# Kernel tuning notes

Measured on AMD Instinct MI355X. Metric: run time of the kernel, lower is better.

## Reference

```python
import jax, jax.numpy as jnp
import numpy as np

DIM = 384
HEADS = 6
HD = DIM // HEADS
PATCH = 2
FR = 0.5
HEXP = int(HEADS * 4.0)       # attn_proj expanded heads
PR = DIM // 4                  # SQA proj1 out dim
HID = DIM * 4                  # MLP hidden
EPS = 1e-5
SCALE = 1.0 / np.sqrt(HD).astype(np.float32)


def _ln(x, w, b):
    m = jnp.mean(x, axis=-1, keepdims=True)
    v = jnp.var(x, axis=-1, keepdims=True)
    return (x - m) / jnp.sqrt(v + EPS) * w + b


def _lin(x, w, b):
    return x @ w.T + b


def setup_inputs() -> dict:
    key = jax.random.key(0)
    ks = jax.random.split(key, 16)
    def p(i, shape, s=0.02):
        return jax.random.normal(ks[i], shape, jnp.float32) * s
    return {
        "x": jax.random.normal(ks[0], (3136, DIM), jnp.float32),
        "qa": jax.random.normal(ks[1], (1, DIM), jnp.float32),
        "conv_w": p(2, (DIM, 1, 3, 3), 0.1),
        "conv_b": jnp.zeros((DIM,), jnp.float32),
        "norm1_w": jnp.ones((DIM,), jnp.float32),
        "norm1_b": jnp.zeros((DIM,), jnp.float32),
        "norm2_w": jnp.ones((DIM,), jnp.float32),
        "norm2_b": jnp.zeros((DIM,), jnp.float32),
        "qkv_w": p(3, (3 * DIM, DIM)),
        "qkv_b": jnp.zeros((3 * DIM,), jnp.float32),
        "mproj_w": p(4, (DIM, DIM)),
        "mproj_b": jnp.zeros((DIM,), jnp.float32),
        "ap1_w": p(5, (HEXP, HEADS), 0.1),
        "ap1_b": jnp.zeros((HEXP,), jnp.float32),
        "ap2_w": p(6, (HEADS, HEXP), 0.1),
        "ap2_b": jnp.zeros((HEADS,), jnp.float32),
        "kv_w": p(7, (2 * DIM, DIM)),
        "kv_b": jnp.zeros((2 * DIM,), jnp.float32),
        "sp1_w": p(8, (PR, DIM)),
        "sp1_b": jnp.zeros((PR,), jnp.float32),
        "sp2_w": p(9, (DIM, PR)),
        "sp2_b": jnp.zeros((DIM,), jnp.float32),
        "pn_w": jnp.ones((PR,), jnp.float32),
        "pn_b": jnp.zeros((PR,), jnp.float32),
        "fc1_w": p(10, (HID, DIM)),
        "fc1_b": jnp.zeros((HID,), jnp.float32),
        "fc2_w": p(11, (DIM, HID)),
        "fc2_b": jnp.zeros((DIM,), jnp.float32),
    }


def _mmsa(x, qkv_w, qkv_b, mproj_w, mproj_b, ap1_w, ap1_b, ap2_w, ap2_b):
    # x: [S, DIM]
    s = x.shape[0]
    qkv = _lin(x, qkv_w, qkv_b).reshape(s, 3, HEADS, HD).transpose(1, 2, 0, 3)  # [3,h,s,d]
    q, k, v = qkv[0], qkv[1], qkv[2]
    attn = jnp.einsum('hqd,hkd->hqk', q, k) * SCALE           # [h,q,k]
    a = attn.transpose(1, 2, 0)                                # [q,k,h]
    a = a @ ap1_w.T + ap1_b                                    # [q,k,hexp]
    a = jax.nn.softmax(a, axis=1)                              # softmax over k (axis=1)
    a = a @ ap2_w.T + ap2_b                                    # [q,k,h]
    attn = a.transpose(2, 0, 1)                                # [h,q,k]
    out = jnp.einsum('hqk,hkd->hqd', attn, v)
    out = out.transpose(1, 0, 2).reshape(s, DIM)
    return _lin(out, mproj_w, mproj_b)


def _sqa(x, q, kv_w, kv_b, sp1_w, sp1_b, sp2_w, sp2_b, pn_w, pn_b):
    # x: [S, DIM], q: [1, DIM]
    s = x.shape[0]
    qh = q.reshape(1, HEADS, HD).transpose(1, 0, 2)            # [h,1,d]
    kv = _lin(x, kv_w, kv_b).reshape(s, 2, HEADS, HD).transpose(1, 2, 0, 3)
    k, v = kv[0], kv[1]
    attn = jax.nn.softmax(jnp.einsum('hqd,hkd->hqk', qh, k) * SCALE, axis=-1)
    x1 = jnp.einsum('hqk,hkd->hqd', attn, v).transpose(1, 0, 2).reshape(1, DIM)
    x1 = jax.nn.relu(_ln(_lin(x1, sp1_w, sp1_b), pn_w, pn_b))
    x1 = _lin(x1, sp2_w, sp2_b)
    return x + x1                                              # broadcast residual over S


def reference(x, qa, conv_w, conv_b, norm1_w, norm1_b, norm2_w, norm2_b,
              qkv_w, qkv_b, mproj_w, mproj_b, ap1_w, ap1_b, ap2_w, ap2_b,
              kv_w, kv_b, sp1_w, sp1_b, sp2_w, sp2_b, pn_w, pn_b,
              fc1_w, fc1_b, fc2_w, fc2_b):
    L = x.shape[0]
    Hs = int(np.sqrt(L)); Ws = Hs
    # PosCNN2D: depthwise 3x3 conv + residual
    xi = x.T.reshape(1, DIM, Hs, Ws)
    conv = jax.lax.conv_general_dilated(xi, conv_w, (1, 1), 'SAME', feature_group_count=DIM)
    xi = conv + conv_b[None, :, None, None] + xi
    c = xi[0]                                                  # [DIM,Hs,Ws]
    hp, wp = Hs // PATCH, Ws // PATCH
    # 'c (h h1) (w w1) -> (h w) (h1 w1) c'
    x1 = c.reshape(DIM, hp, PATCH, wp, PATCH).transpose(1, 3, 2, 4, 0).reshape(hp * wp, PATCH * PATCH, DIM)
    n = hp * wp
    nf = int(n * FR)
    means = x1.mean(axis=(1, 2))
    idx = jnp.argsort(-means)                                  # descending
    nf_idx, nb_idx = idx[:nf], idx[nf:]
    f = x1[nf_idx].reshape(nf * PATCH * PATCH, DIM)
    b = x1[nb_idx].reshape((n - nf) * PATCH * PATCH, DIM)
    qf = _mmsa(jnp.concatenate([qa, f], axis=0),
               qkv_w, qkv_b, mproj_w, mproj_b, ap1_w, ap1_b, ap2_w, ap2_b)
    qa2, f = qf[:1], qf[1:]
    b = _sqa(b, qa2, kv_w, kv_b, sp1_w, sp1_b, sp2_w, sp2_b, pn_w, pn_b)
    # scatter foreground/background back to patch order
    x1n = jnp.zeros_like(x1)
    x1n = x1n.at[nf_idx].set(f.reshape(nf, PATCH * PATCH, DIM))
    x1n = x1n.at[nb_idx].set(b.reshape(n - nf, PATCH * PATCH, DIM))
    # inverse rearrange '(h w) (h1 w1) c -> ((h h1)(w w1)) c'
    x1f = x1n.reshape(hp, wp, PATCH, PATCH, DIM).transpose(0, 2, 1, 3, 4).reshape(L, DIM)
    x = x + _ln(x1f, norm1_w, norm1_b)
    h = _ln(x, norm2_w, norm2_b)
    h = jax.nn.silu(_lin(h, fc1_w, fc1_b))
    x = x + _lin(h, fc2_w, fc2_b)
    return x, qa2
```

## Files before the change

### kernel.cpp

```cpp
#include <hip/hip_runtime.h>
#include <hip/hip_bf16.h>

#define DIM 384
#define HEADS 6
#define HD 64
#define LPIX 3136
#define HS 56
#define NPATCH 784
#define NF 392
#define SEQ 1569
#define BROWS 1568
#define HEXP 24
#define PR 96
#define HID 1536
#define SCALE 0.125f
#define EPSV 1e-5f
#define KPAD 1576
#define QSTR 9456

typedef short short8v __attribute__((ext_vector_type(8)));
typedef float f32x4 __attribute__((ext_vector_type(4)));
typedef unsigned short ushort;

__device__ __forceinline__ ushort f2b(float f) {
    __hip_bfloat16 h = __float2bfloat16(f);
    return reinterpret_cast<ushort&>(h);
}
__device__ __forceinline__ float b2f(ushort u) {
    unsigned int ui = ((unsigned int)u) << 16;
    return __uint_as_float(ui);
}

struct CvtSeg { const float* s; ushort* d; int n; };
__global__ __launch_bounds__(256) void cvt_kernel(CvtSeg a, CvtSeg b, CvtSeg c, CvtSeg d, CvtSeg e) {
    CvtSeg seg;
    switch (blockIdx.y) { case 0: seg = a; break; case 1: seg = b; break; case 2: seg = c; break;
                          case 3: seg = d; break; default: seg = e; break; }
    int idx = (blockIdx.x * 256 + threadIdx.x) * 8;
    if (idx >= seg.n) return;
    float4 f0 = *reinterpret_cast<const float4*>(seg.s + idx);
    float4 f1 = *reinterpret_cast<const float4*>(seg.s + idx + 4);
    ushort u[8] = { f2b(f0.x), f2b(f0.y), f2b(f0.z), f2b(f0.w),
                    f2b(f1.x), f2b(f1.y), f2b(f1.z), f2b(f1.w) };
    *reinterpret_cast<uint4*>(seg.d + idx) = *reinterpret_cast<uint4*>(u);
}

__global__ __launch_bounds__(384) void conv_kernel(const float* __restrict__ x,
                                                   const float* __restrict__ cw,
                                                   const float* __restrict__ cb,
                                                   float* __restrict__ x1,
                                                   float* __restrict__ means) {
    int l = blockIdx.x, c = threadIdx.x;
    int wid = c >> 6, lane = c & 63;
    int hh = l / HS, ww = l % HS;
    float acc = x[(long)l * DIM + c] + cb[c];
    #pragma unroll
    for (int kh = 0; kh < 3; kh++) {
        int h2 = hh + kh - 1;
        if (h2 < 0 || h2 >= HS) continue;
        #pragma unroll
        for (int kw = 0; kw < 3; kw++) {
            int w2 = ww + kw - 1;
            if (w2 < 0 || w2 >= HS) continue;
            acc += x[((long)h2 * HS + w2) * DIM + c] * cw[c * 9 + kh * 3 + kw];
        }
    }
    int p = (hh >> 1) * 28 + (ww >> 1);
    int t = ((hh & 1) << 1) | (ww & 1);
    x1[(long)(p * 4 + t) * DIM + c] = acc;
    float s = acc;
    #pragma unroll
    for (int off = 32; off >= 1; off >>= 1) s += __shfl_xor(s, off);
    __shared__ float wred[6];
    if (lane == 0) wred[wid] = s;
    __syncthreads();
    if (c == 0) atomicAdd(&means[p], wred[0] + wred[1] + wred[2] + wred[3] + wred[4] + wred[5]);
}

__global__ __launch_bounds__(1024) void partition_kernel(const float* __restrict__ means, int* __restrict__ isfg,
                                                         int* __restrict__ pos, int* __restrict__ fgmap,
                                                         int* __restrict__ bgmap) {
    __shared__ float m_s[NPATCH];
    __shared__ unsigned char flag_s[NPATCH];
    __shared__ int scan_s[256];
    int tid = threadIdx.x;
    if (tid < NPATCH) m_s[tid] = means[tid];
    __syncthreads();
    if (tid < NPATCH) {
        float m = m_s[tid];
        int rank = 0;
        for (int q2 = 0; q2 < NPATCH; q2++) {
            float mq = m_s[q2];
            rank += (mq > m) || (mq == m && q2 < tid);
        }
        flag_s[tid] = (rank < NF) ? 1 : 0;
    }
    __syncthreads();
    if (tid < 256) {
        int base = tid * 4, cnt = 0;
        #pragma unroll
        for (int i = 0; i < 4; i++) { int p = base + i; if (p < NPATCH) cnt += flag_s[p]; }
        scan_s[tid] = cnt;
    }
    __syncthreads();
    for (int off = 1; off < 256; off <<= 1) {
        int add = 0;
        if (tid < 256 && tid >= off) add = scan_s[tid - off];
        __syncthreads();
        if (tid < 256) scan_s[tid] += add;
        __syncthreads();
    }
    if (tid < 256) {
        int base = tid * 4, cnt = 0;
        #pragma unroll
        for (int i = 0; i < 4; i++) { int p = base + i; if (p < NPATCH) cnt += flag_s[p]; }
        int run = scan_s[tid] - cnt;
        for (int i = 0; i < 4; i++) {
            int p = base + i;
            if (p >= NPATCH) break;
            int f = flag_s[p];
            if (f) { isfg[p] = 1; pos[p] = run; fgmap[run] = p; run++; }
            else   { isfg[p] = 0; pos[p] = p - run; bgmap[p - run] = p; }
        }
    }
}

__global__ __launch_bounds__(384) void gather_kernel(const float* __restrict__ x1, const float* __restrict__ qa,
                                                     const int* __restrict__ fgmap, const int* __restrict__ bgmap,
                                                     ushort* __restrict__ Xmsa_bf, float* __restrict__ B,
                                                     ushort* __restrict__ B_bf) {
    int c = threadIdx.x;
    int bid = blockIdx.x;
    if (bid == 0) { Xmsa_bf[c] = f2b(qa[c]); return; }
    if (bid <= BROWS) {
        int r = bid - 1;
        int src = fgmap[r >> 2] * 4 + (r & 3);
        Xmsa_bf[(long)bid * DIM + c] = f2b(x1[(long)src * DIM + c]);
    } else {
        int r = bid - SEQ;
        int src = bgmap[r >> 2] * 4 + (r & 3);
        float v = x1[(long)src * DIM + c];
        B[(long)r * DIM + c] = v;
        B_bf[(long)r * DIM + c] = f2b(v);
    }
}

template<int BM, int BN, int BK, int OPB, int ACT, int OUTBF>
__global__ __launch_bounds__(256) void mgemm(
    const ushort* __restrict__ A, int lda, long long sA,
    const ushort* __restrict__ B, int ldb, long long sB,
    const float* __restrict__ bias, const float* __restrict__ resid, int ldr,
    void* __restrict__ Cv, int ldc, long long sC,
    int M, int N, int K, float alpha) {
    constexpr int LDT = BK + 8;
    constexpr int WR = (BM == 128 && BN == 128) ? 2 : ((BM == 128) ? 4 : 2);
    constexpr int WC = 4 / WR;
    constexpr int MFR = BM / WR / 16;
    constexpr int NFR = BN / WC / 16;
    constexpr int KH = BK / 32;
    __shared__ ushort As[BM * LDT];
    __shared__ ushort Bs[BN * LDT];
    int tid = threadIdx.x;
    int wid = tid >> 6, lane = tid & 63;
    int m0 = blockIdx.y * BM, n0 = blockIdx.x * BN;
    int bz = blockIdx.z;
    A += (long long)bz * sA;
    B += (long long)bz * sB;
    int wm = (wid / WC) * (BM / WR);
    int wn = (wid % WC) * (BN / WC);
    f32x4 acc[MFR][NFR];
    #pragma unroll
    for (int mi = 0; mi < MFR; mi++)
        #pragma unroll
        for (int ni = 0; ni < NFR; ni++) acc[mi][ni] = (f32x4){0.f, 0.f, 0.f, 0.f};

    for (int k0 = 0; k0 < K; k0 += BK) {
        {
            constexpr int CPR = BK / 8;
            constexpr int CHA = BM * CPR / 256;
            #pragma unroll
            for (int t = 0; t < CHA; t++) {
                int chunk = tid + t * 256;
                int row = chunk / CPR, part = chunk % CPR;
                int gm = m0 + row, gk = k0 + part * 8;
                ushort* dst = &As[row * LDT + part * 8];
                if (gm < M && gk + 8 <= K) {
                    *reinterpret_cast<uint4*>(dst) =
                        *reinterpret_cast<const uint4*>(&A[(long long)gm * lda + gk]);
                } else {
                    #pragma unroll
                    for (int i = 0; i < 8; i++) {
                        int k = gk + i;
                        dst[i] = (gm < M && k < K) ? A[(long long)gm * lda + k] : (ushort)0;
                    }
                }
            }
        }
        if (OPB == 1) {
            constexpr int CPR = BK / 8;
            constexpr int CHB = BN * CPR / 256;
            #pragma unroll
            for (int t = 0; t < CHB; t++) {
                int chunk = tid + t * 256;
                int row = chunk / CPR, part = chunk % CPR;
                int gn = n0 + row, gk = k0 + part * 8;
                ushort* dst = &Bs[row * LDT + part * 8];
                if (gn < N && gk + 8 <= K) {
                    *reinterpret_cast<uint4*>(dst) =
                        *reinterpret_cast<const uint4*>(&B[(long long)gn * ldb + gk]);
                } else {
                    #pragma unroll
                    for (int i = 0; i < 8; i++) {
                        int k = gk + i;
                        dst[i] = (gn < N && k < K) ? B[(long long)gn * ldb + k] : (ushort)0;
                    }
                }
            }
        } else {
            int kr = tid >> 2, nn = (tid & 3) * 16;
            int gk = k0 + kr;
            ushort vals[16];
            if (gk < K && n0 + nn + 16 <= N) {
                *reinterpret_cast<uint4*>(vals) =
                    *reinterpret_cast<const uint4*>(&B[(long long)gk * ldb + n0 + nn]);
                *reinterpret_cast<uint4*>(vals + 8) =
                    *reinterpret_cast<const uint4*>(&B[(long long)gk * ldb + n0 + nn + 8]);
            } else {
                #pragma unroll
                for (int i = 0; i < 16; i++) {
                    int gn = n0 + nn + i;
                    vals[i] = (gk < K && gn < N) ? B[(long long)gk * ldb + gn] : (ushort)0;
                }
            }
            #pragma unroll
            for (int i = 0; i < 16; i++) Bs[(nn + i) * LDT + kr] = vals[i];
        }
        __syncthreads();
        #pragma unroll
        for (int kh = 0; kh < KH; kh++) {
            short8v a[MFR], b[NFR];
            int kcol = kh * 32 + (lane >> 4) * 8;
            #pragma unroll
            for (int mi = 0; mi < MFR; mi++)
                a[mi] = *reinterpret_cast<const short8v*>(&As[(wm + mi * 16 + (lane & 15)) * LDT + kcol]);
            #pragma unroll
            for (int ni = 0; ni < NFR; ni++)
                b[ni] = *reinterpret_cast<const short8v*>(&Bs[(wn + ni * 16 + (lane & 15)) * LDT + kcol]);
            #pragma unroll
            for (int mi = 0; mi < MFR; mi++)
                #pragma unroll
                for (int ni = 0; ni < NFR; ni++)
                    acc[mi][ni] = __builtin_amdgcn_mfma_f32_16x16x32_bf16(a[mi], b[ni], acc[mi][ni], 0, 0, 0);
        }
        __syncthreads();
    }
    ushort* C16 = (ushort*)Cv;
    float* C32 = (float*)Cv;
    #pragma unroll
    for (int mi = 0; mi < MFR; mi++) {
        #pragma unroll
        for (int j = 0; j < 4; j++) {
            int gm = m0 + wm + mi * 16 + (lane >> 4) * 4 + j;
            if (gm >= M) continue;
            #pragma unroll
            for (int ni = 0; ni < NFR; ni++) {
                int gn = n0 + wn + ni * 16 + (lane & 15);
                if (gn >= N) continue;
                float v = acc[mi][ni][j] * alpha;
                if (bias) v += bias[gn];
                if (ACT == 1) v = v / (1.f + __expf(-v));
                if (resid) v += resid[(long long)gm * ldr + gn];
                long long ci = bz * sC + (long long)gm * ldc + gn;
                if (OUTBF) C16[ci] = f2b(v); else C32[ci] = v;
            }
        }
    }
}

__global__ __launch_bounds__(512, 2) void modattn_kernel(
    ushort* __restrict__ S,
    const float* __restrict__ ap1_w, const float* __restrict__ ap1_b,
    const float* __restrict__ ap2_w, const float* __restrict__ ap2_b) {
    int q = blockIdx.x, tid = threadIdx.x;
    int wid = tid >> 6, lane = tid & 63;
    __shared__ ushort s_lds[6 * KPAD];
    __shared__ float w1s[144], w2s[144], b1s[24], b2s[6];
    __shared__ float red[8][12];
    __shared__ float fin[12];
    if (tid < 144) { w1s[tid] = ap1_w[tid]; w2s[tid] = ap2_w[tid]; }
    if (tid < 24) b1s[tid] = ap1_b[tid];
    if (tid < 6)  b2s[tid] = ap2_b[tid];
    {
        const uint4* g = reinterpret_cast<const uint4*>(S + (long long)q * QSTR);
        uint4* l = reinterpret_cast<uint4*>(s_lds);
        #pragma unroll
        for (int t = 0; t < 3; t++) {
            int i = tid + t * 512;
            if (i < 1182) l[i] = g[i];
        }
    }
    __syncthreads();
    float a2acc[4][6];
    #pragma unroll
    for (int j = 0; j < 4; j++)
        #pragma unroll
        for (int h = 0; h < 6; h++) a2acc[j][h] = b2s[h];

    #pragma unroll
    for (int c = 0; c < 2; c++) {
        float a1[4][12];
        float r12[12];
        #pragma unroll
        for (int e = 0; e < 12; e++) r12[e] = -3.4e38f;
        #pragma unroll
        for (int j = 0; j < 4; j++) {
            int k = tid + j * 512;
            bool val = k < SEQ;
            int kc = val ? k : 0;
            float sv[6];
            #pragma unroll
            for (int h = 0; h < 6; h++) sv[h] = b2f(s_lds[h * KPAD + kc]);
            #pragma unroll
            for (int e = 0; e < 12; e++) {
                int eg = c * 12 + e;
                float a = b1s[eg];
                #pragma unroll
                for (int h = 0; h < 6; h++) a = fmaf(sv[h], w1s[eg * 6 + h], a);
                a1[j][e] = a;
                if (val) r12[e] = fmaxf(r12[e], a);
            }
        }
        #pragma unroll
        for (int e = 0; e < 12; e++) {
            float v = r12[e];
            #pragma unroll
            for (int off = 32; off >= 1; off >>= 1) v = fmaxf(v, __shfl_xor(v, off));
            r12[e] = v;
        }
        if (lane == 0) {
            #pragma unroll
            for (int e = 0; e < 12; e++) red[wid][e] = r12[e];
        }
        __syncthreads();
        if (tid < 12) {
            float v = red[0][tid];
            #pragma unroll
            for (int w = 1; w < 8; w++) v = fmaxf(v, red[w][tid]);
            fin[tid] = v;
        }
        __syncthreads();
        #pragma unroll
        for (int e = 0; e < 12; e++) r12[e] = 0.f;
        #pragma unroll
        for (int j = 0; j < 4; j++) {
            int k = tid + j * 512;
            bool val = k < SEQ;
            #pragma unroll
            for (int e = 0; e < 12; e++) {
                float p = val ? __expf(a1[j][e] - fin[e]) : 0.f;
                a1[j][e] = p;
                r12[e] += p;
            }
        }
        #pragma unroll
        for (int e = 0; e < 12; e++) {
            float v = r12[e];
            #pragma unroll
            for (int off = 32; off >= 1; off >>= 1) v += __shfl_xor(v, off);
            r12[e] = v;
        }
        if (lane == 0) {
            #pragma unroll
            for (int e = 0; e < 12; e++) red[wid][e] = r12[e];
        }
        __syncthreads();
        if (tid < 12) {
            float v = red[0][tid];
            #pragma unroll
            for (int w = 1; w < 8; w++) v += red[w][tid];
            fin[tid] = 1.f / v;
        }
        __syncthreads();
        #pragma unroll
        for (int j = 0; j < 4; j++) {
            #pragma unroll
            for (int e = 0; e < 12; e++) {
                float p = a1[j][e] * fin[e];
                int eg = c * 12 + e;
                #pragma unroll
                for (int h = 0; h < 6; h++) a2acc[j][h] = fmaf(p, w2s[h * 24 + eg], a2acc[j][h]);
            }
        }
    }
    #pragma unroll
    for (int j = 0; j < 4; j++) {
        int k = tid + j * 512;
        if (k < SEQ) {
            #pragma unroll
            for (int h = 0; h < 6; h++) s_lds[h * KPAD + k] = f2b(a2acc[j][h]);
        } else if (k < KPAD) {
            #pragma unroll
            for (int h = 0; h < 6; h++) s_lds[h * KPAD + k] = 0;
        }
    }
    __syncthreads();
    {
        const uint4* l = reinterpret_cast<const uint4*>(s_lds);
        uint4* g = reinterpret_cast<uint4*>(S + (long long)q * QSTR);
        #pragma unroll
        for (int t = 0; t < 3; t++) {
            int i = tid + t * 512;
            if (i < 1182) g[i] = l[i];
        }
    }
}

__global__ __launch_bounds__(512) void sqa_attn_kernel(const float* __restrict__ kv, const float* __restrict__ qa2,
                                                       float* __restrict__ x1h) {
    int h = blockIdx.x, tid = threadIdx.x;
    int wid = tid >> 6, lane = tid & 63;
    __shared__ float q_s[HD];
    __shared__ float l_s[BROWS];
    __shared__ float red8[8];
    __shared__ float pvred[8][HD];
    __shared__ float gmv;
    if (tid < HD) q_s[tid] = qa2[h * HD + tid];
    __syncthreads();
    float lmax = -1e30f;
    #pragma unroll
    for (int j = 0; j < 4; j++) {
        int s = tid + j * 512;
        if (s < BROWS) {
            const float4* kr = reinterpret_cast<const float4*>(kv + (long long)s * 768 + h * HD);
            float d = 0.f;
            #pragma unroll
            for (int i = 0; i < 16; i++) {
                float4 f = kr[i];
                d = fmaf(f.x, q_s[i * 4 + 0], d); d = fmaf(f.y, q_s[i * 4 + 1], d);
                d = fmaf(f.z, q_s[i * 4 + 2], d); d = fmaf(f.w, q_s[i * 4 + 3], d);
            }
            d *= SCALE;
            l_s[s] = d;
            lmax = fmaxf(lmax, d);
        }
    }
    #pragma unroll
    for (int off = 32; off >= 1; off >>= 1) lmax = fmaxf(lmax, __shfl_xor(lmax, off));
    if (lane == 0) red8[wid] = lmax;
    __syncthreads();
    if (tid == 0) {
        float v = red8[0];
        #pragma unroll
        for (int w = 1; w < 8; w++) v = fmaxf(v, red8[w]);
        gmv = v;
    }
    __syncthreads();
    float gmax = gmv;
    float lsum = 0.f;
    #pragma unroll
    for (int j = 0; j < 4; j++) {
        int s = tid + j * 512;
        if (s < BROWS) { float p = __expf(l_s[s] - gmax); l_s[s] = p; lsum += p; }
    }
    #pragma unroll
    for (int off = 32; off >= 1; off >>= 1) lsum += __shfl_xor(lsum, off);
    if (lane == 0) red8[wid] = lsum;
    __syncthreads();
    if (tid == 0) {
        float v = 0.f;
        #pragma unroll
        for (int w = 0; w < 8; w++) v += red8[w];
        gmv = 1.f / v;
    }
    __syncthreads();
    float inv = gmv;
    int d = tid & 63, g = tid >> 6;
    float acc = 0.f;
    for (int s = g; s < BROWS; s += 8)
        acc = fmaf(l_s[s], kv[(long long)s * 768 + 384 + h * HD + d], acc);
    pvred[g][d] = acc;
    __syncthreads();
    if (tid < HD) {
        float v = 0.f;
        #pragma unroll
        for (int w = 0; w < 8; w++) v += pvred[w][tid];
        x1h[h * HD + tid] = v * inv;
    }
}

__global__ __launch_bounds__(384) void sqa_mlp_kernel(const float* __restrict__ x1h,
                                                      const float* __restrict__ sp1_w, const float* __restrict__ sp1_b,
                                                      const float* __restrict__ pn_w, const float* __restrict__ pn_b,
                                                      const float* __restrict__ sp2_w, const float* __restrict__ sp2_b,
                                                      float* __restrict__ z,
                                                      const float* __restrict__ mp, float* __restrict__ dq) {
    __shared__ float y_s[PR];
    __shared__ float x_s[DIM];
    __shared__ float mv[2];
    int tid = threadIdx.x;
    dq[tid] = mp[tid];
    x_s[tid] = x1h[tid];
    __syncthreads();
    if (tid < PR) {
        float a = sp1_b[tid];
        for (int c = 0; c < DIM; c++) a += sp1_w[tid * DIM + c] * x_s[c];
        y_s[tid] = a;
    }
    __syncthreads();
    if (tid == 0) {
        float m = 0.f; for (int i = 0; i < PR; i++) m += y_s[i]; m /= (float)PR;
        float v = 0.f; for (int i = 0; i < PR; i++) { float d = y_s[i] - m; v += d * d; } v /= (float)PR;
        mv[0] = m; mv[1] = rsqrtf(v + EPSV);
    }
    __syncthreads();
    if (tid < PR) {
        float yn = (y_s[tid] - mv[0]) * mv[1] * pn_w[tid] + pn_b[tid];
        y_s[tid] = fmaxf(yn, 0.f);
    }
    __syncthreads();
    float a = sp2_b[tid];
    for (int j = 0; j < PR; j++) a += sp2_w[tid * PR + j] * y_s[j];
    z[tid] = a;
}

__global__ __launch_bounds__(384) void scatter_ln_kernel(
    const float* __restrict__ x, const float* __restrict__ mpout, const float* __restrict__ B,
    const float* __restrict__ z, const int* __restrict__ isfg, const int* __restrict__ pos,
    const float* __restrict__ n1w, const float* __restrict__ n1b,
    const float* __restrict__ n2w, const float* __restrict__ n2b,
    float* __restrict__ x_mid, ushort* __restrict__ hnorm_bf) {
    int l = blockIdx.x, c = threadIdx.x;
    int wid = c >> 6, lane = c & 63;
    int hh = l / HS, ww = l % HS;
    int p = (hh >> 1) * 28 + (ww >> 1);
    int t = ((hh & 1) << 1) | (ww & 1);
    float v;
    if (isfg[p]) v = mpout[(long long)(1 + pos[p] * 4 + t) * DIM + c];
    else v = B[(long long)(pos[p] * 4 + t) * DIM + c] + z[c];
    __shared__ float r0[8], r1[8], r2[8], r3[8];
    float s1 = v, s2 = v * v;
    #pragma unroll
    for (int off = 32; off >= 1; off >>= 1) { s1 += __shfl_xor(s1, off); s2 += __shfl_xor(s2, off); }
    if (lane == 0) { r0[wid] = s1; r1[wid] = s2; }
    __syncthreads();
    float mean = (r0[0] + r0[1] + r0[2] + r0[3] + r0[4] + r0[5]) / (float)DIM;
    float var = (r1[0] + r1[1] + r1[2] + r1[3] + r1[4] + r1[5]) / (float)DIM - mean * mean;
    float xm = x[(long long)l * DIM + c] + (v - mean) * rsqrtf(var + EPSV) * n1w[c] + n1b[c];
    x_mid[(long long)l * DIM + c] = xm;
    s1 = xm; s2 = xm * xm;
    #pragma unroll
    for (int off = 32; off >= 1; off >>= 1) { s1 += __shfl_xor(s1, off); s2 += __shfl_xor(s2, off); }
    if (lane == 0) { r2[wid] = s1; r3[wid] = s2; }
    __syncthreads();
    float m2 = (r2[0] + r2[1] + r2[2] + r2[3] + r2[4] + r2[5]) / (float)DIM;
    float v2 = (r3[0] + r3[1] + r3[2] + r3[3] + r3[4] + r3[5]) / (float)DIM - m2 * m2;
    hnorm_bf[(long long)l * DIM + c] = f2b((xm - m2) * rsqrtf(v2 + EPSV) * n2w[c] + n2b[c]);
}

extern "C" void kernel_launch(void* const* d_in, const int* in_sizes, int n_in,
                              void* d_out, int out_size, void* d_ws, size_t ws_size,
                              hipStream_t stream) {
    const float* x       = (const float*)d_in[0];
    const float* qa      = (const float*)d_in[1];
    const float* conv_w  = (const float*)d_in[2];
    const float* conv_b  = (const float*)d_in[3];
    const float* n1w     = (const float*)d_in[4];
    const float* n1b     = (const float*)d_in[5];
    const float* n2w     = (const float*)d_in[6];
    const float* n2b     = (const float*)d_in[7];
    const float* qkv_w   = (const float*)d_in[8];
    const float* qkv_b   = (const float*)d_in[9];
    const float* mproj_w = (const float*)d_in[10];
    const float* mproj_b = (const float*)d_in[11];
    const float* ap1_w   = (const float*)d_in[12];
    const float* ap1_b   = (const float*)d_in[13];
    const float* ap2_w   = (const float*)d_in[14];
    const float* ap2_b   = (const float*)d_in[15];
    const float* kv_w    = (const float*)d_in[16];
    const float* kv_b    = (const float*)d_in[17];
    const float* sp1_w   = (const float*)d_in[18];
    const float* sp1_b   = (const float*)d_in[19];
    const float* sp2_w   = (const float*)d_in[20];
    const float* sp2_b   = (const float*)d_in[21];
    const float* pn_w    = (const float*)d_in[22];
    const float* pn_b    = (const float*)d_in[23];
    const float* fc1_w   = (const float*)d_in[24];
    const float* fc1_b   = (const float*)d_in[25];
    const float* fc2_w   = (const float*)d_in[26];
    const float* fc2_b   = (const float*)d_in[27];
    float* out = (float*)d_out;
    float* ws  = (float*)d_ws;

    const long long X1_OFF    = 0;
    const long long BMAT_OFF  = 1204224;
    const long long S_OFF     = 1806336;
    const long long MPOUT_OFF = 16576912;
    const long long XMID_OFF  = 17179408;
    const long long WBF_OFF   = 18383632;
    const long long MEANS_OFF = 19415824;
    const long long X1H_OFF   = 19416608;
    const long long Z_OFF     = 19416992;
    const long long ISFG_OFF  = 19418160;
    const long long POS_OFF   = 19418944;
    const long long FGMAP_OFF = 19419728;
    const long long BGMAP_OFF = 19420120;

    float*  x1_arr  = ws + X1_OFF;
    float*  Bmat    = ws + BMAT_OFF;
    float*  mpout   = ws + MPOUT_OFF;
    float*  xmid    = ws + XMID_OFF;
    float*  means   = ws + MEANS_OFF;
    float*  x1h     = ws + X1H_OFF;
    float*  zvec    = ws + Z_OFF;
    int*    isfg    = (int*)(ws + ISFG_OFF);
    int*    pos     = (int*)(ws + POS_OFF);
    int*    fgmap   = (int*)(ws + FGMAP_OFF);
    int*    bgmap   = (int*)(ws + BGMAP_OFF);

    ushort* S16     = (ushort*)(ws + S_OFF);
    ushort* qkvb_bf = (ushort*)(ws + X1_OFF);
    ushort* Xmsa_bf = (ushort*)(ws + MPOUT_OFF);
    ushort* Bmat_bf = (ushort*)(ws + XMID_OFF);
    ushort* attn_bf = (ushort*)(ws + XMID_OFF + 301056);
    float*  kv_out  = ws + S_OFF;
    ushort* hnorm_bf= (ushort*)(ws + S_OFF + 1204224);
    ushort* hact_bf = (ushort*)(ws + S_OFF + 1806336);

    ushort* wbf      = (ushort*)(ws + WBF_OFF);
    ushort* qkvw_bf  = wbf;
    ushort* mprojw_bf= wbf + 442368;
    ushort* kvw_bf   = wbf + 589824;
    ushort* fc1w_bf  = wbf + 884736;
    ushort* fc2w_bf  = wbf + 1474560;

    {
        CvtSeg s0{qkv_w, qkvw_bf, 442368};
        CvtSeg s1{mproj_w, mprojw_bf, 147456};
        CvtSeg s2{kv_w, kvw_bf, 294912};
        CvtSeg s3{fc1_w, fc1w_bf, 589824};
        CvtSeg s4{fc2_w, fc2w_bf, 589824};
        dim3 g(288, 5, 1);
        cvt_kernel<<<g, 256, 0, stream>>>(s0, s1, s2, s3, s4);
    }

    hipMemsetAsync(means, 0, NPATCH * sizeof(float), stream);
    conv_kernel<<<LPIX, 384, 0, stream>>>(x, conv_w, conv_b, x1_arr, means);
    partition_kernel<<<1, 1024, 0, stream>>>(means, isfg, pos, fgmap, bgmap);
    gather_kernel<<<SEQ + BROWS, 384, 0, stream>>>(x1_arr, qa, fgmap, bgmap, Xmsa_bf, Bmat, Bmat_bf);

    {
        dim3 g(18, 25, 1);
        mgemm<64,64,64,1,0,1><<<g, 256, 0, stream>>>(Xmsa_bf, DIM, 0, qkvw_bf, DIM, 0, qkv_b,
                                                     nullptr, 0, qkvb_bf, 1152, 0, SEQ, 1152, DIM, 1.f);
    }
    {
        dim3 g(13, 13, 6);
        mgemm<128,128,64,1,0,1><<<g, 256, 0, stream>>>(qkvb_bf, 1152, 64, qkvb_bf + 384, 1152, 64, nullptr,
                                                       nullptr, 0, S16, QSTR, (long long)KPAD, SEQ, SEQ, HD, SCALE);
    }
    modattn_kernel<<<SEQ, 512, 0, stream>>>(S16, ap1_w, ap1_b, ap2_w, ap2_b);
    {
        dim3 g(1, 25, 6);
        mgemm<64,64,64,0,0,1><<<g, 256, 0, stream>>>(S16, QSTR, (long long)KPAD, qkvb_bf + 768, 1152, 64, nullptr,
                                                     nullptr, 0, attn_bf, DIM, 64, SEQ, HD, SEQ, 1.f);
    }
    {
        dim3 g(6, 25, 1);
        mgemm<64,64,64,1,0,0><<<g, 256, 0, stream>>>(attn_bf, DIM, 0, mprojw_bf, DIM, 0, mproj_b,
                                                     nullptr, 0, mpout, DIM, 0, SEQ, DIM, DIM, 1.f);
    }
    {
        dim3 g(12, 25, 1);
        mgemm<64,64,64,1,0,0><<<g, 256, 0, stream>>>(Bmat_bf, DIM, 0, kvw_bf, DIM, 0, kv_b,
                                                     nullptr, 0, kv_out, 768, 0, BROWS, 768, DIM, 1.f);
    }
    sqa_attn_kernel<<<HEADS, 512, 0, stream>>>(kv_out, mpout , x1h);
    sqa_mlp_kernel<<<1, 384, 0, stream>>>(x1h, sp1_w, sp1_b, pn_w, pn_b, sp2_w, sp2_b, zvec,
                                          mpout, out + (long long)LPIX * DIM);
    scatter_ln_kernel<<<LPIX, 384, 0, stream>>>(x, mpout, Bmat, zvec, isfg, pos,
                                                n1w, n1b, n2w, n2b, xmid, hnorm_bf);
    {
        dim3 g(12, 25, 1);
        mgemm<128,128,64,1,1,1><<<g, 256, 0, stream>>>(hnorm_bf, DIM, 0, fc1w_bf, DIM, 0, fc1_b,
                                                       nullptr, 0, hact_bf, HID, 0, LPIX, HID, DIM, 1.f);
    }
    {
        dim3 g(6, 50, 1);
        mgemm<64,64,64,1,0,0><<<g, 256, 0, stream>>>(hact_bf, HID, 0, fc2w_bf, HID, 0, fc2_b,
                                                     xmid, DIM, out, DIM, 0, LPIX, DIM, HID, 1.f);
    }
}
```

Baseline: 557.9 us.

## Split modattn expanded heads across waves and drop fp32 background copy

The modulated-attention kernel is restructured so each wave owns 3 of the 24 expanded heads and loops over all keys. This replaces block-wide shared-memory reductions and barriers with wave-level shuffles, and per-head contributions are combined through LDS float atomics into a zeroed buffer. Separately, the fp32 copy of the background rows is no longer written; the scatter/LayerNorm kernel reads the bf16 copy instead, which saves memory traffic but lowers precision of the residual path. The atomics and the larger register array (75 floats per thread) may cost occupancy or contention.

```diff
diff --git a/kernel.cpp b/kernel.cpp
--- a/kernel.cpp
+++ b/kernel.cpp
@@ -30,6 +30,8 @@
     unsigned int ui = ((unsigned int)u) << 16;
     return __uint_as_float(ui);
 }
+__device__ __forceinline__ float b2f_lo(unsigned int u) { return __uint_as_float(u << 16); }
+__device__ __forceinline__ float b2f_hi(unsigned int u) { return __uint_as_float(u & 0xffff0000u); }
 
 struct CvtSeg { const float* s; ushort* d; int n; };
 __global__ __launch_bounds__(256) void cvt_kernel(CvtSeg a, CvtSeg b, CvtSeg c, CvtSeg d, CvtSeg e) {
@@ -127,8 +129,7 @@
 
 __global__ __launch_bounds__(384) void gather_kernel(const float* __restrict__ x1, const float* __restrict__ qa,
                                                      const int* __restrict__ fgmap, const int* __restrict__ bgmap,
-                                                     ushort* __restrict__ Xmsa_bf, float* __restrict__ B,
-                                                     ushort* __restrict__ B_bf) {
+                                                     ushort* __restrict__ Xmsa_bf, ushort* __restrict__ B_bf) {
     int c = threadIdx.x;
     int bid = blockIdx.x;
     if (bid == 0) { Xmsa_bf[c] = f2b(qa[c]); return; }
@@ -139,9 +140,7 @@
     } else {
         int r = bid - SEQ;
         int src = bgmap[r >> 2] * 4 + (r & 3);
-        float v = x1[(long)src * DIM + c];
-        B[(long)r * DIM + c] = v;
-        B_bf[(long)r * DIM + c] = f2b(v);
+        B_bf[(long)r * DIM + c] = f2b(x1[(long)src * DIM + c]);
     }
 }
 
@@ -282,130 +281,121 @@
     const float* __restrict__ ap1_w, const float* __restrict__ ap1_b,
     const float* __restrict__ ap2_w, const float* __restrict__ ap2_b) {
     int q = blockIdx.x, tid = threadIdx.x;
-    int wid = tid >> 6, lane = tid & 63;
-    __shared__ ushort s_lds[6 * KPAD];
+    int wv = tid >> 6, lane = tid & 63;
+    __shared__ unsigned int sk32[3 * KPAD];
+    __shared__ float a2buf[6 * KPAD];
     __shared__ float w1s[144], w2s[144], b1s[24], b2s[6];
-    __shared__ float red[8][12];
-    __shared__ float fin[12];
     if (tid < 144) { w1s[tid] = ap1_w[tid]; w2s[tid] = ap2_w[tid]; }
     if (tid < 24) b1s[tid] = ap1_b[tid];
     if (tid < 6)  b2s[tid] = ap2_b[tid];
     {
+        uint4* z = reinterpret_cast<uint4*>(a2buf);
+        uint4 zero = {0, 0, 0, 0};
+        #pragma unroll
+        for (int t = 0; t < 5; t++) { int i = tid + t * 512; if (i < 2364) z[i] = zero; }
+    }
+    {
         const uint4* g = reinterpret_cast<const uint4*>(S + (long long)q * QSTR);
-        uint4* l = reinterpret_cast<uint4*>(s_lds);
+        ushort* sku = reinterpret_cast<ushort*>(sk32);
         #pragma unroll
         for (int t = 0; t < 3; t++) {
             int i = tid + t * 512;
-            if (i < 1182) l[i] = g[i];
-        }
-    }
-    __syncthreads();
-    float a2acc[4][6];
-    #pragma unroll
-    for (int j = 0; j < 4; j++)
-        #pragma unroll
-        for (int h = 0; h < 6; h++) a2acc[j][h] = b2s[h];
-
-    #pragma unroll
-    for (int c = 0; c < 2; c++) {
-        float a1[4][12];
-        float r12[12];
-        #pragma unroll
-        for (int e = 0; e < 12; e++) r12[e] = -3.4e38f;
-        #pragma unroll
-        for (int j = 0; j < 4; j++) {
-            int k = tid + j * 512;
-            bool val = k < SEQ;
-            int kc = val ? k : 0;
-            float sv[6];
-            #pragma unroll
-            for (int h = 0; h < 6; h++) sv[h] = b2f(s_lds[h * KPAD + kc]);
-            #pragma unroll
-            for (int e = 0; e < 12; e++) {
-                int eg = c * 12 + e;
-                float a = b1s[eg];
+            if (i < 1182) {
+                uint4 v = g[i];
+                int h = i / 197;
+                int k0 = (i - h * 197) * 8;
+                int base = (h >> 1) * 2 * KPAD + (h & 1);
+                ushort u[8];
+                *reinterpret_cast<uint4*>(u) = v;
                 #pragma unroll
-                for (int h = 0; h < 6; h++) a = fmaf(sv[h], w1s[eg * 6 + h], a);
-                a1[j][e] = a;
-                if (val) r12[e] = fmaxf(r12[e], a);
+                for (int x2 = 0; x2 < 8; x2++) sku[base + 2 * (k0 + x2)] = u[x2];
             }
         }
-        #pragma unroll
-        for (int e = 0; e < 12; e++) {
-            float v = r12[e];
-            #pragma unroll
-            for (int off = 32; off >= 1; off >>= 1) v = fmaxf(v, __shfl_xor(v, off));
-            r12[e] = v;
-        }
-        if (lane == 0) {
-            #pragma unroll
-            for (int e = 0; e < 12; e++) red[wid][e] = r12[e];
-        }
-        __syncthreads();
-        if (tid < 12) {
-            float v = red[0][tid];
-            #pragma unroll
-            for (int w = 1; w < 8; w++) v = fmaxf(v, red[w][tid]);
-            fin[tid] = v;
-        }
-        __syncthreads();
-        #pragma unroll
-        for (int e = 0; e < 12; e++) r12[e] = 0.f;
-        #pragma unroll
-        for (int j = 0; j < 4; j++) {
-            int k = tid + j * 512;
-            bool val = k < SEQ;
-            #pragma unroll
-            for (int e = 0; e < 12; e++) {
-                float p = val ? __expf(a1[j][e] - fin[e]) : 0.f;
-                a1[j][e] = p;
-                r12[e] += p;
-            }
-        }
-        #pragma unroll
-        for (int e = 0; e < 12; e++) {
-            float v = r12[e];
-            #pragma unroll
-            for (int off = 32; off >= 1; off >>= 1) v += __shfl_xor(v, off);
-            r12[e] = v;
-        }
-        if (lane == 0) {
-            #pragma unroll
-            for (int e = 0; e < 12; e++) red[wid][e] = r12[e];
-        }
-        __syncthreads();
-        if (tid < 12) {
-            float v = red[0][tid];
-            #pragma unroll
-            for (int w = 1; w < 8; w++) v += red[w][tid];
-            fin[tid] = 1.f / v;
-        }
-        __syncthreads();
-        #pragma unroll
-        for (int j = 0; j < 4; j++) {
-            #pragma unroll
-            for (int e = 0; e < 12; e++) {
-                float p = a1[j][e] * fin[e];
-                int eg = c * 12 + e;
-                #pragma unroll
-                for (int h = 0; h < 6; h++) a2acc[j][h] = fmaf(p, w2s[h * 24 + eg], a2acc[j][h]);
-            }
-        }
-    }
+    }
+    __syncthreads();
+    int e0 = wv * 3;
+    int kl = (lane + wv * 8) & 63;
+    float w1a[3][6], b1a[3];
+    #pragma unroll
+    for (int e = 0; e < 3; e++) {
+        b1a[e] = b1s[e0 + e];
+        #pragma unroll
+        for (int h = 0; h < 6; h++) w1a[e][h] = w1s[(e0 + e) * 6 + h];
+    }
+    float p[25][3];
+    float mx0 = -3.4e38f, mx1 = -3.4e38f, mx2 = -3.4e38f;
+    #pragma unroll
+    for (int j = 0; j < 25; j++) {
+        int k = kl + j * 64;
+        bool val = k < SEQ;
+        int kc = val ? k : 0;
+        unsigned int u01 = sk32[kc], u23 = sk32[KPAD + kc], u45 = sk32[2 * KPAD + kc];
+        float sv[6] = { b2f_lo(u01), b2f_hi(u01), b2f_lo(u23), b2f_hi(u23), b2f_lo(u45), b2f_hi(u45) };
+        #pragma unroll
+        for (int e = 0; e < 3; e++) {
+            float a = b1a[e];
+            #pragma unroll
+            for (int h = 0; h < 6; h++) a = fmaf(sv[h], w1a[e][h], a);
+            p[j][e] = a;
+        }
+        if (val) { mx0 = fmaxf(mx0, p[j][0]); mx1 = fmaxf(mx1, p[j][1]); mx2 = fmaxf(mx2, p[j][2]); }
+    }
+    #pragma unroll
+    for (int off = 32; off >= 1; off >>= 1) {
+        mx0 = fmaxf(mx0, __shfl_xor(mx0, off));
+        mx1 = fmaxf(mx1, __shfl_xor(mx1, off));
+        mx2 = fmaxf(mx2, __shfl_xor(mx2, off));
+    }
+    float s0 = 0.f, s1 = 0.f, s2 = 0.f;
+    #pragma unroll
+    for (int j = 0; j < 25; j++) {
+        int k = kl + j * 64;
+        bool val = k < SEQ;
+        float p0 = val ? __expf(p[j][0] - mx0) : 0.f;
+        float p1 = val ? __expf(p[j][1] - mx1) : 0.f;
+        float p2 = val ? __expf(p[j][2] - mx2) : 0.f;
+        p[j][0] = p0; p[j][1] = p1; p[j][2] = p2;
+        s0 += p0; s1 += p1; s2 += p2;
+    }
+    #pragma unroll
+    for (int off = 32; off >= 1; off >>= 1) {
+        s0 += __shfl_xor(s0, off);
+        s1 += __shfl_xor(s1, off);
+        s2 += __shfl_xor(s2, off);
+    }
+    float i0 = 1.f / s0, i1 = 1.f / s1, i2 = 1.f / s2;
+    float w2a[6][3];
+    #pragma unroll
+    for (int h = 0; h < 6; h++)
+        #pragma unroll
+        for (int e = 0; e < 3; e++) w2a[h][e] = w2s[h * 24 + e0 + e];
+    #pragma unroll
+    for (int j = 0; j < 25; j++) {
+        int k = kl + j * 64;
+        if (k >= SEQ) continue;
+        float p0 = p[j][0] * i0, p1 = p[j][1] * i1, p2 = p[j][2] * i2;
+        #pragma unroll
+        for (int h = 0; h < 6; h++) {
+            float v = p0 * w2a[h][0] + p1 * w2a[h][1] + p2 * w2a[h][2];
+            atomicAdd(&a2buf[h * KPAD + k], v);
+        }
+    }
+    __syncthreads();
+    ushort* osk = reinterpret_cast<ushort*>(sk32);
     #pragma unroll
     for (int j = 0; j < 4; j++) {
         int k = tid + j * 512;
-        if (k < SEQ) {
-            #pragma unroll
-            for (int h = 0; h < 6; h++) s_lds[h * KPAD + k] = f2b(a2acc[j][h]);
-        } else if (k < KPAD) {
-            #pragma unroll
-            for (int h = 0; h < 6; h++) s_lds[h * KPAD + k] = 0;
-        }
-    }
-    __syncthreads();
-    {
-        const uint4* l = reinterpret_cast<const uint4*>(s_lds);
+        if (k >= KPAD) break;
+        bool val = k < SEQ;
+        #pragma unroll
+        for (int h = 0; h < 6; h++) {
+            float v = val ? (a2buf[h * KPAD + k] + b2s[h]) : 0.f;
+            osk[h * KPAD + k] = f2b(v);
+        }
+    }
+    __syncthreads();
+    {
+        const uint4* l = reinterpret_cast<const uint4*>(osk);
         uint4* g = reinterpret_cast<uint4*>(S + (long long)q * QSTR);
         #pragma unroll
         for (int t = 0; t < 3; t++) {
@@ -460,7 +450,7 @@
     #pragma unroll
     for (int j = 0; j < 4; j++) {
         int s = tid + j * 512;
-        if (s < BROWS) { float p = __expf(l_s[s] - gmax); l_s[s] = p; lsum += p; }
+        if (s < BROWS) { float pp = __expf(l_s[s] - gmax); l_s[s] = pp; lsum += pp; }
     }
     #pragma unroll
     for (int off = 32; off >= 1; off >>= 1) lsum += __shfl_xor(lsum, off);
@@ -524,7 +514,7 @@
 }
 
 __global__ __launch_bounds__(384) void scatter_ln_kernel(
-    const float* __restrict__ x, const float* __restrict__ mpout, const float* __restrict__ B,
+    const float* __restrict__ x, const float* __restrict__ mpout, const ushort* __restrict__ B_bf,
     const float* __restrict__ z, const int* __restrict__ isfg, const int* __restrict__ pos,
     const float* __restrict__ n1w, const float* __restrict__ n1b,
     const float* __restrict__ n2w, const float* __restrict__ n2b,
@@ -536,7 +526,7 @@
     int t = ((hh & 1) << 1) | (ww & 1);
     float v;
     if (isfg[p]) v = mpout[(long long)(1 + pos[p] * 4 + t) * DIM + c];
-    else v = B[(long long)(pos[p] * 4 + t) * DIM + c] + z[c];
+    else v = b2f(B_bf[(long long)(pos[p] * 4 + t) * DIM + c]) + z[c];
     __shared__ float r0[8], r1[8], r2[8], r3[8];
     float s1 = v, s2 = v * v;
     #pragma unroll
@@ -606,7 +596,6 @@
     const long long BGMAP_OFF = 19420120;
 
     float*  x1_arr  = ws + X1_OFF;
-    float*  Bmat    = ws + BMAT_OFF;
     float*  mpout   = ws + MPOUT_OFF;
     float*  xmid    = ws + XMID_OFF;
     float*  means   = ws + MEANS_OFF;
@@ -620,8 +609,8 @@
     ushort* S16     = (ushort*)(ws + S_OFF);
     ushort* qkvb_bf = (ushort*)(ws + X1_OFF);
     ushort* Xmsa_bf = (ushort*)(ws + MPOUT_OFF);
-    ushort* Bmat_bf = (ushort*)(ws + XMID_OFF);
-    ushort* attn_bf = (ushort*)(ws + XMID_OFF + 301056);
+    ushort* Bmat_bf = (ushort*)(ws + BMAT_OFF);
+    ushort* attn_bf = (ushort*)(ws + XMID_OFF);
     float*  kv_out  = ws + S_OFF;
     ushort* hnorm_bf= (ushort*)(ws + S_OFF + 1204224);
     ushort* hact_bf = (ushort*)(ws + S_OFF + 1806336);
@@ -646,7 +635,7 @@
     hipMemsetAsync(means, 0, NPATCH * sizeof(float), stream);
     conv_kernel<<<LPIX, 384, 0, stream>>>(x, conv_w, conv_b, x1_arr, means);
     partition_kernel<<<1, 1024, 0, stream>>>(means, isfg, pos, fgmap, bgmap);
-    gather_kernel<<<SEQ + BROWS, 384, 0, stream>>>(x1_arr, qa, fgmap, bgmap, Xmsa_bf, Bmat, Bmat_bf);
+    gather_kernel<<<SEQ + BROWS, 384, 0, stream>>>(x1_arr, qa, fgmap, bgmap, Xmsa_bf, Bmat_bf);
 
     {
         dim3 g(18, 25, 1);
@@ -677,7 +666,7 @@
     sqa_attn_kernel<<<HEADS, 512, 0, stream>>>(kv_out, mpout , x1h);
     sqa_mlp_kernel<<<1, 384, 0, stream>>>(x1h, sp1_w, sp1_b, pn_w, pn_b, sp2_w, sp2_b, zvec,
                                           mpout, out + (long long)LPIX * DIM);
-    scatter_ln_kernel<<<LPIX, 384, 0, stream>>>(x, mpout, Bmat, zvec, isfg, pos,
+    scatter_ln_kernel<<<LPIX, 384, 0, stream>>>(x, mpout, Bmat_bf, zvec, isfg, pos,
                                                 n1w, n1b, n2w, n2b, xmid, hnorm_bf);
     {
         dim3 g(12, 25, 1);
```

Measured after the change: 1.160 ms. 108% more time.
